# Kernel tuning notes

Hardware: AMD Instinct MI355X
Metric: run time of the kernel (lower is better)

Reference implementation:

```python
import jax, jax.numpy as jnp
import numpy as np
import math

B, L, IN, HID, NLAYERS, AA = 16, 512, 512, 512, 6, 21
KAPPA_ADD = 5.0


def _sru_layer(x, W, v, b):
    # x: [L, B, din]; W: [din, 2*HID*k]; v, b: [2(gate f/r), 2(dir), HID]
    Lx, Bx, din = x.shape
    d = HID
    k = W.shape[1] // (2 * d)  # 4 if projecting residual, 3 if residual = input
    U = (x @ W).reshape(Lx, Bx, 2, d, k)
    res = U[..., 3] if k == 4 else x.reshape(Lx, Bx, 2, d)
    # time-flip direction 1 so a single scan handles both directions
    flip = lambda a: jnp.concatenate([a[:, :, :1], a[::-1, :, 1:]], axis=2)
    u0, u1, u2, resf = flip(U[..., 0]), flip(U[..., 1]), flip(U[..., 2]), flip(res)
    vf, vr = v[0], v[1]
    bf, br = b[0], b[1]

    def step(c, t):
        u0t, u1t, u2t, rt = t
        f = jax.nn.sigmoid(u1t + vf * c + bf)
        c1 = f * c + (1.0 - f) * u0t
        r = jax.nn.sigmoid(u2t + vr * c1 + br)
        h = r * c1 + (1.0 - r) * rt
        return c1, h

    c0 = jnp.zeros((Bx, 2, d), x.dtype)
    _, H = jax.lax.scan(step, c0, (u0, u1, u2, resf))
    return flip(H).reshape(Lx, Bx, 2 * d)


def setup_inputs():
    key = jax.random.key(0)
    inp = {}
    inp['input'] = jax.random.normal(jax.random.fold_in(key, 0), (B, L, IN), jnp.float32)
    inp['hidden'] = jnp.zeros((NLAYERS, B, 2 * HID), jnp.float32)
    for l in range(NLAYERS):
        din = IN if l == 0 else 2 * HID
        k = 4 if din != 2 * HID else 3
        inp[f'sru_w{l}'] = jax.random.normal(jax.random.fold_in(key, 10 + l), (din, 2 * HID * k), jnp.float32) * (1.0 / math.sqrt(din))
        inp[f'sru_v{l}'] = jax.random.normal(jax.random.fold_in(key, 20 + l), (2, 2, HID), jnp.float32) * 0.1
        inp[f'sru_b{l}'] = jnp.zeros((2, 2, HID), jnp.float32)

    def lin(seed, din, dout):
        w = jax.random.normal(jax.random.fold_in(key, seed), (din, dout), jnp.float32) * (1.0 / math.sqrt(din))
        return w, jnp.zeros((dout,), jnp.float32)

    inp['fc1_logits_w'], inp['fc1_logits_b'] = lin(30, 2 * HID, HID)
    inp['fc2_logits_w'], inp['fc2_logits_b'] = lin(31, HID, AA)
    inp['fc1_angles_w'], inp['fc1_angles_b'] = lin(32, 2 * HID, HID)
    inp['fc2_means_w'], inp['fc2_means_b'] = lin(33, HID, 2)
    inp['fc2_kappas_w'], inp['fc2_kappas_b'] = lin(34, HID, 2)
    return inp


def reference(input, hidden, sru_w0, sru_v0, sru_b0, sru_w1, sru_v1, sru_b1, sru_w2, sru_v2, sru_b2, sru_w3, sru_v3, sru_b3, sru_w4, sru_v4, sru_b4, sru_w5, sru_v5, sru_b5, fc1_logits_w, fc1_logits_b, fc2_logits_w, fc2_logits_b, fc1_angles_w, fc1_angles_b, fc2_means_w, fc2_means_b, fc2_kappas_w, fc2_kappas_b):
    x = input.transpose(1, 0, 2)  # [L, B, IN]
    ws = [sru_w0, sru_w1, sru_w2, sru_w3, sru_w4, sru_w5]
    vs = [sru_v0, sru_v1, sru_v2, sru_v3, sru_v4, sru_v5]
    bs = [sru_b0, sru_b1, sru_b2, sru_b3, sru_b4, sru_b5]
    for W, v, b in zip(ws, vs, bs):
        x = _sru_layer(x, W, v, b)
    sru_out = x.transpose(1, 0, 2)  # [B, L, 2*HID]
    h_log = sru_out @ fc1_logits_w + fc1_logits_b
    output_logits = jax.nn.log_softmax(h_log @ fc2_logits_w + fc2_logits_b, axis=-1)
    h_ang = sru_out @ fc1_angles_w + fc1_angles_b
    output_means = jnp.tanh(h_ang @ fc2_means_w + fc2_means_b) * math.pi
    output_kappas = KAPPA_ADD + jax.nn.softplus(h_ang @ fc2_kappas_w + fc2_kappas_b)
    return (output_logits, output_means, output_kappas)
```

## Files before the change

### kernel.cpp

```cpp
#include <hip/hip_runtime.h>

typedef __attribute__((ext_vector_type(8))) short short8;
typedef __attribute__((ext_vector_type(4))) float f32x4;

__device__ __forceinline__ ushort f2bf(float x) {
  unsigned u = __builtin_bit_cast(unsigned, x);
  u = (u + 0x7fffu + ((u >> 16) & 1u)) >> 16;
  return (ushort)u;
}
__device__ __forceinline__ float bf2f(ushort x) {
  return __builtin_bit_cast(float, ((unsigned)x) << 16);
}

#define AS1CP(p) ((const __attribute__((address_space(1))) unsigned int*)(p))
#define AS3CP(p) ((__attribute__((address_space(3))) unsigned int*)(p))
#define GLDS(g, l, SZ) __builtin_amdgcn_global_load_lds(AS1CP(g), AS3CP(l), SZ, 0, 0)

__global__ __launch_bounds__(256) void k_cvt(const float* __restrict__ in,
                                             ushort* __restrict__ out, int n4) {
  int i = blockIdx.x * 256 + threadIdx.x;
  if (i >= n4) return;
  float4 v = reinterpret_cast<const float4*>(in)[i];
  ushort4 o;
  o.x = f2bf(v.x); o.y = f2bf(v.y); o.z = f2bf(v.z); o.w = f2bf(v.w);
  reinterpret_cast<ushort4*>(out)[i] = o;
}

__global__ __launch_bounds__(256) void k_transpose(const float* __restrict__ W,
                                                   ushort* __restrict__ Wt,
                                                   int N, int K) {
  __shared__ float tile[32][33];
  int bx = blockIdx.x * 32;
  int by = blockIdx.y * 32;
  int tx = threadIdx.x, ty = threadIdx.y;
#pragma unroll
  for (int i = 0; i < 32; i += 8)
    tile[ty + i][tx] = W[(size_t)(by + ty + i) * N + bx + tx];
  __syncthreads();
#pragma unroll
  for (int i = 0; i < 32; i += 8)
    Wt[(size_t)(bx + ty + i) * K + by + tx] = f2bf(tile[tx][ty + i]);
}

template <int BF16OUT>
__global__ __launch_bounds__(256) void k_gemm(const ushort* __restrict__ A,
                                              const ushort* __restrict__ Bt,
                                              void* __restrict__ Cv,
                                              int K, int N) {
  __shared__ __align__(16) ushort lsA[2][4096];
  __shared__ __align__(16) ushort lsB[2][4096];
  const int tid = threadIdx.x;
  const int bm = blockIdx.x, bn = blockIdx.y;
  const int w = tid >> 6, l = tid & 63;
  const int wm = (w >> 1) * 64, wn = (w & 1) * 64;
  const int lr = l & 15, lg = l >> 4;
  f32x4 acc[4][4] = {};
  const int srow = tid >> 2;
  const int scol = (((tid & 3) ^ ((srow >> 1) & 3))) * 8;
  const ushort* Ag = A + (size_t)(bm * 128 + srow) * K + scol;
  const ushort* Bg = Bt + (size_t)(bn * 128 + srow) * K + scol;
  const int nt = K >> 5;
  const int rxor = (lr >> 1) & 3;

#define GEMM_ISSUE(BUF, KT)                                       \
  {                                                               \
    GLDS(Ag + (KT), &lsA[BUF][w * 512], 16);                      \
    GLDS(Ag + (size_t)64 * K + (KT), &lsA[BUF][2048 + w * 512], 16); \
    GLDS(Bg + (KT), &lsB[BUF][w * 512], 16);                      \
    GLDS(Bg + (size_t)64 * K + (KT), &lsB[BUF][2048 + w * 512], 16); \
  }

  GEMM_ISSUE(0, 0);
  for (int t = 0; t < nt; ++t) {
    const int cur = t & 1;
    if (t + 1 < nt) {
      GEMM_ISSUE(cur ^ 1, (t + 1) * 32);
      asm volatile("s_waitcnt vmcnt(4)" ::: "memory");
    } else {
      asm volatile("s_waitcnt vmcnt(0)" ::: "memory");
    }
    asm volatile("s_barrier" ::: "memory");
    short8 af[4], bfr[4];
#pragma unroll
    for (int i = 0; i < 4; ++i)
      af[i] = *(const short8*)&lsA[cur][(wm + i * 16 + lr) * 32 + ((lg ^ rxor) * 8)];
#pragma unroll
    for (int j = 0; j < 4; ++j)
      bfr[j] = *(const short8*)&lsB[cur][(wn + j * 16 + lr) * 32 + ((lg ^ rxor) * 8)];
#pragma unroll
    for (int i = 0; i < 4; ++i)
#pragma unroll
      for (int j = 0; j < 4; ++j)
        acc[i][j] = __builtin_amdgcn_mfma_f32_16x16x32_bf16(af[i], bfr[j], acc[i][j], 0, 0, 0);
    asm volatile("s_barrier" ::: "memory");
  }
#undef GEMM_ISSUE
  const size_t cbase = (size_t)(bm * 128 + wm + lg * 4) * N + bn * 128 + wn + lr;
  if (BF16OUT) {
    ushort* Cb = (ushort*)Cv + cbase;
#pragma unroll
    for (int i = 0; i < 4; ++i)
#pragma unroll
      for (int j = 0; j < 4; ++j)
#pragma unroll
        for (int r = 0; r < 4; ++r)
          Cb[(size_t)(i * 16 + r) * N + j * 16] = f2bf(acc[i][j][r]);
  } else {
    float* Cb = (float*)Cv + cbase;
#pragma unroll
    for (int i = 0; i < 4; ++i)
#pragma unroll
      for (int j = 0; j < 4; ++j)
#pragma unroll
        for (int r = 0; r < 4; ++r)
          Cb[(size_t)(i * 16 + r) * N + j * 16] = acc[i][j][r];
  }
}

template <int KK>
__global__ __launch_bounds__(64, 1) void sru_rec5(const float* __restrict__ U,
                                                  const ushort* __restrict__ Xres,
                                                  const float* __restrict__ v,
                                                  const float* __restrict__ bb,
                                                  ushort* __restrict__ H) {
  const int lane = threadIdx.x;
  if (lane >= 16) return;
  const int blk = blockIdx.x;
  const int b = blk >> 6, rem = blk & 63, dir = rem >> 5, c0 = (rem & 31) << 4;
  const int h = c0 + lane;
  const float vf = v[dir * 512 + h], vr = v[1024 + dir * 512 + h];
  const float bfv = bb[dir * 512 + h], brv = bb[1024 + dir * 512 + h];
  const float vfn = -vf, vrn = -vr;
  const float kf0 = -bfv, kr0 = -brv;
  const int rs = 1024 * KK;
  const int tstep = dir ? -1 : 1;
  const int t0 = dir ? 511 : 0;
  const float* Ub = U + (size_t)b * 512 * rs + dir * 512 * KK + (size_t)h * KK;
  const ushort* Xb = Xres + (size_t)b * 512 * 1024 + dir * 512 + h;
  ushort* Hb = H + (size_t)b * 512 * 1024 + dir * 512 + h;

  float4 r4[4][8];
  float3 r3[4][8];
  ushort xr[4][8];

#define SR_ISSUE(J, TI)                                                        \
  {                                                                            \
    const int base_ = (TI) * 8;                                                \
    _Pragma("unroll")                                                          \
    for (int t = 0; t < 8; ++t) {                                              \
      int tt = t0 + tstep * (base_ + t);                                       \
      if (KK == 4) {                                                           \
        r4[J][t] = *(const float4*)(Ub + (size_t)tt * rs);                     \
      } else {                                                                 \
        r3[J][t] = *(const float3*)(Ub + (size_t)tt * rs);                     \
        xr[J][t] = Xb[(size_t)tt * 1024];                                      \
      }                                                                        \
    }                                                                          \
  }

#define SR_COMP(J, TI)                                                         \
  {                                                                            \
    _Pragma("unroll")                                                          \
    for (int s = 0; s < 8; ++s) {                                              \
      float u0, u1, u2, uR;                                                    \
      if (KK == 4) {                                                           \
        u0 = r4[J][s].x; u1 = r4[J][s].y; u2 = r4[J][s].z; uR = r4[J][s].w;    \
      } else {                                                                 \
        u0 = r3[J][s].x; u1 = r3[J][s].y; u2 = r3[J][s].z; uR = bf2f(xr[J][s]);\
      }                                                                        \
      float ef = __expf(__builtin_fmaf(vfn, c, kf0 - u1));                     \
      float f = __builtin_amdgcn_rcpf(1.f + ef);                               \
      c = __builtin_fmaf(f, c - u0, u0);                                       \
      float er = __expf(__builtin_fmaf(vrn, c, kr0 - u2));                     \
      float r = __builtin_amdgcn_rcpf(1.f + er);                               \
      float hh = __builtin_fmaf(r, c - uR, uR);                                \
      Hb[(size_t)(t0 + tstep * ((TI) * 8 + s)) * 1024] = f2bf(hh);             \
    }                                                                          \
  }

#define SR_WAIT                                                                \
  {                                                                            \
    if (KK == 3) asm volatile("s_waitcnt vmcnt(32)" ::: "memory");             \
    else         asm volatile("s_waitcnt vmcnt(16)" ::: "memory");             \
  }

  SR_ISSUE(0, 0)
  SR_ISSUE(1, 1)
  SR_ISSUE(2, 2)

  float c = 0.f;
#pragma unroll 1
  for (int ii = 0; ii < 15; ++ii) {
#define TILE_J(J)                                                              \
    {                                                                          \
      const int i = ii * 4 + (J);                                              \
      SR_WAIT                                                                  \
      SR_ISSUE((((J) + 3) & 3), i + 3)                                         \
      SR_COMP(J, i)                                                            \
    }
    TILE_J(0) TILE_J(1) TILE_J(2) TILE_J(3)
#undef TILE_J
  }
  SR_WAIT SR_ISSUE(3, 63) SR_COMP(0, 60)
  SR_WAIT SR_COMP(1, 61)
  SR_WAIT SR_COMP(2, 62)
  asm volatile("s_waitcnt vmcnt(0)" ::: "memory");
  SR_COMP(3, 63)
#undef SR_ISSUE
#undef SR_COMP
#undef SR_WAIT
}

__global__ __launch_bounds__(256) void k_buildW2(const float* __restrict__ w2l,
                                                 const float* __restrict__ w2m,
                                                 const float* __restrict__ w2k,
                                                 ushort* __restrict__ Wt2) {
  int i = blockIdx.x * 256 + threadIdx.x;
  if (i >= 128 * 1024) return;
  int n = i >> 10, k = i & 1023;
  float vv = 0.f;
  if (n < 21 && k < 512) vv = w2l[k * 21 + n];
  else if (n >= 21 && n < 23 && k >= 512) vv = w2m[(k - 512) * 2 + (n - 21)];
  else if (n >= 23 && n < 25 && k >= 512) vv = w2k[(k - 512) * 2 + (n - 23)];
  Wt2[i] = f2bf(vv);
}

__global__ __launch_bounds__(64) void k_bias25(const float* __restrict__ b1l,
                                               const float* __restrict__ b1a,
                                               const float* __restrict__ w2l,
                                               const float* __restrict__ b2l,
                                               const float* __restrict__ w2m,
                                               const float* __restrict__ b2m,
                                               const float* __restrict__ w2k,
                                               const float* __restrict__ b2k,
                                               float* __restrict__ b2adj) {
  int o = threadIdx.x;
  if (o >= 25) return;
  float s;
  if (o < 21) {
    s = b2l[o];
    for (int k = 0; k < 512; ++k) s += b1l[k] * w2l[k * 21 + o];
  } else if (o < 23) {
    s = b2m[o - 21];
    for (int k = 0; k < 512; ++k) s += b1a[k] * w2m[k * 2 + (o - 21)];
  } else {
    s = b2k[o - 23];
    for (int k = 0; k < 512; ++k) s += b1a[k] * w2k[k * 2 + (o - 23)];
  }
  b2adj[o] = s;
}

__global__ __launch_bounds__(64) void k_act(const float* __restrict__ T,
                                            const float* __restrict__ b2adj,
                                            float* __restrict__ out) {
  const int row = blockIdx.x;
  const int lane = threadIdx.x;
  float myv = 0.f;
  if (lane < 25) myv = T[(size_t)row * 128 + lane] + b2adj[lane];
  float x = (lane < 21) ? myv : -1e30f;
#pragma unroll
  for (int off = 32; off; off >>= 1) x = fmaxf(x, __shfl_xor(x, off));
  float e = (lane < 21) ? expf(myv - x) : 0.f;
#pragma unroll
  for (int off = 32; off; off >>= 1) e += __shfl_xor(e, off);
  float lse = x + logf(e);
  if (lane < 21) {
    out[(size_t)row * 21 + lane] = myv - lse;
  } else if (lane < 23) {
    out[172032 + row * 2 + (lane - 21)] = tanhf(myv) * 3.14159265358979323846f;
  } else if (lane < 25) {
    float sp = (myv > 20.f) ? myv : log1pf(expf(myv));
    out[188416 + row * 2 + (lane - 23)] = 5.f + sp;
  }
}

extern "C" void kernel_launch(void* const* d_in, const int* in_sizes, int n_in,
                              void* d_out, int out_size, void* d_ws, size_t ws_size,
                              hipStream_t stream) {
  (void)in_sizes; (void)n_in; (void)out_size; (void)ws_size;
  const float* input = (const float*)d_in[0];
  const float* sw[6]; const float* sv[6]; const float* sb[6];
  for (int l = 0; l < 6; ++l) {
    sw[l] = (const float*)d_in[2 + 3 * l];
    sv[l] = (const float*)d_in[3 + 3 * l];
    sb[l] = (const float*)d_in[4 + 3 * l];
  }
  const float* fc1lw = (const float*)d_in[20];
  const float* fc1lb = (const float*)d_in[21];
  const float* fc2lw = (const float*)d_in[22];
  const float* fc2lb = (const float*)d_in[23];
  const float* fc1aw = (const float*)d_in[24];
  const float* fc1ab = (const float*)d_in[25];
  const float* fc2mw = (const float*)d_in[26];
  const float* fc2mb = (const float*)d_in[27];
  const float* fc2kw = (const float*)d_in[28];
  const float* fc2kb = (const float*)d_in[29];

  char* ws = (char*)d_ws;
  float* U = (float*)ws;
  ushort* Hcat2 = (ushort*)ws;
  float* T = (float*)(ws + 67108864);
  ushort* H0 = (ushort*)(ws + 134217728);
  ushort* H1 = (ushort*)(ws + 150994944);
  ushort* X0 = (ushort*)(ws + 167772160);
  const size_t wbase = 176160768;
  ushort* Wtl[6];
  Wtl[0] = (ushort*)(ws + wbase);
  for (int l = 1; l < 6; ++l)
    Wtl[l] = (ushort*)(ws + wbase + 4194304 + (size_t)(l - 1) * 6291456);
  ushort* Wfc = (ushort*)(ws + wbase + 4194304 + 5ull * 6291456);
  ushort* Wt2 = (ushort*)(ws + wbase + 37748736);
  float* b2adj = (float*)(ws + wbase + 38010880);

  k_cvt<<<4096, 256, 0, stream>>>(input, X0, 8192 * 512 / 4);
  k_buildW2<<<512, 256, 0, stream>>>(fc2lw, fc2mw, fc2kw, Wt2);
  k_bias25<<<1, 64, 0, stream>>>(fc1lb, fc1ab, fc2lw, fc2lb, fc2mw, fc2mb,
                                 fc2kw, fc2kb, b2adj);

  k_transpose<<<dim3(4096 / 32, 512 / 32), dim3(32, 8), 0, stream>>>(sw[0], Wtl[0], 4096, 512);
  for (int l = 1; l < 6; ++l)
    k_transpose<<<dim3(3072 / 32, 1024 / 32), dim3(32, 8), 0, stream>>>(sw[l], Wtl[l], 3072, 1024);
  k_transpose<<<dim3(512 / 32, 1024 / 32), dim3(32, 8), 0, stream>>>(fc1lw, Wfc, 512, 1024);
  k_transpose<<<dim3(512 / 32, 1024 / 32), dim3(32, 8), 0, stream>>>(fc1aw, Wfc + (size_t)512 * 1024, 512, 1024);

  for (int l = 0; l < 6; ++l) {
    const ushort* Ain = (l == 0) ? X0 : ((l & 1) ? H0 : H1);
    ushort* Hout = (l & 1) ? H1 : H0;
    int K = (l == 0) ? 512 : 1024;
    int N = (l == 0) ? 4096 : 3072;
    k_gemm<0><<<dim3(64, N / 128), 256, 0, stream>>>(Ain, Wtl[l], U, K, N);
    if (l == 0)
      sru_rec5<4><<<1024, 64, 0, stream>>>(U, X0 , sv[l], sb[l], Hout);
    else
      sru_rec5<3><<<1024, 64, 0, stream>>>(U, Ain, sv[l], sb[l], Hout);
  }

  k_gemm<1><<<dim3(64, 8), 256, 0, stream>>>(H1, Wfc, Hcat2, 1024, 1024);

  k_gemm<0><<<dim3(64, 1), 256, 0, stream>>>(Hcat2, Wt2, T, 1024, 128);

  k_act<<<8192, 64, 0, stream>>>(T, b2adj, (float*)d_out);
}
```

Measured before the change: 808.5 us.

## Store SRU projections in bf16 with gate-planar column layout and retune prefetch depth

The layer GEMMs now write their U output in bf16 instead of fp32. The weight transpose permutes output columns so u0/u1 sit interleaved, u2 and the residual projection are planar, which lets the recurrence load u0/u1 as one 32-bit word. The recurrence kernel is rewritten to read these bf16 planes, and its prefetch distance drops from three tiles to two. This halves GEMM store and recurrence load traffic, at the cost of bf16 rounding on the pre-activation values and more, smaller load instructions per step.

```diff
diff --git a/kernel.cpp b/kernel.cpp
--- a/kernel.cpp
+++ b/kernel.cpp
@@ -40,6 +40,27 @@
 #pragma unroll
   for (int i = 0; i < 32; i += 8)
     Wt[(size_t)(bx + ty + i) * K + by + tx] = f2bf(tile[tx][ty + i]);
+}
+
+template <int KKp>
+__global__ __launch_bounds__(256) void k_transpose_sru(const float* __restrict__ W,
+                                                       ushort* __restrict__ Wt,
+                                                       int N, int K) {
+  __shared__ float tile[32][33];
+  int bx = blockIdx.x * 32;
+  int by = blockIdx.y * 32;
+  int tx = threadIdx.x, ty = threadIdx.y;
+#pragma unroll
+  for (int i = 0; i < 32; i += 8)
+    tile[ty + i][tx] = W[(size_t)(by + ty + i) * N + bx + tx];
+  __syncthreads();
+#pragma unroll
+  for (int i = 0; i < 32; i += 8) {
+    int c = bx + ty + i;
+    int ch = c / KKp, j = c - ch * KKp;
+    int nc = (j < 2) ? (ch * 2 + j) : ((j == 2) ? (2048 + ch) : (3072 + ch));
+    Wt[(size_t)nc * K + by + tx] = f2bf(tile[tx][ty + i]);
+  }
 }
 
 template <int BF16OUT>
@@ -117,31 +138,29 @@
   }
 }
 
-template <int KK>
-__global__ __launch_bounds__(64, 1) void sru_rec5(const float* __restrict__ U,
-                                                  const ushort* __restrict__ Xres,
+__global__ __launch_bounds__(64, 1) void sru_rec6(const ushort* __restrict__ U, int NU,
+                                                  const ushort* __restrict__ R, int RS,
                                                   const float* __restrict__ v,
                                                   const float* __restrict__ bb,
                                                   ushort* __restrict__ H) {
   const int lane = threadIdx.x;
   if (lane >= 16) return;
   const int blk = blockIdx.x;
-  const int b = blk >> 6, rem = blk & 63, dir = rem >> 5, c0 = (rem & 31) << 4;
-  const int h = c0 + lane;
-  const float vf = v[dir * 512 + h], vr = v[1024 + dir * 512 + h];
-  const float bfv = bb[dir * 512 + h], brv = bb[1024 + dir * 512 + h];
+  const int b = blk >> 6, rem = blk & 63, dir = rem >> 5;
+  const int ch = dir * 512 + ((rem & 31) << 4) + lane;
+  const float vf = v[ch], vr = v[1024 + ch];
+  const float bfv = bb[ch], brv = bb[1024 + ch];
   const float vfn = -vf, vrn = -vr;
   const float kf0 = -bfv, kr0 = -brv;
-  const int rs = 1024 * KK;
   const int tstep = dir ? -1 : 1;
   const int t0 = dir ? 511 : 0;
-  const float* Ub = U + (size_t)b * 512 * rs + dir * 512 * KK + (size_t)h * KK;
-  const ushort* Xb = Xres + (size_t)b * 512 * 1024 + dir * 512 + h;
-  ushort* Hb = H + (size_t)b * 512 * 1024 + dir * 512 + h;
-
-  float4 r4[4][8];
-  float3 r3[4][8];
-  ushort xr[4][8];
+  const ushort* U01 = U + (size_t)b * 512 * NU + ch * 2;
+  const ushort* U2  = U + (size_t)b * 512 * NU + 2048 + ch;
+  const ushort* Rb  = R + (size_t)b * 512 * RS + ch;
+  ushort* Hb = H + (size_t)b * 512 * 1024 + ch;
+
+  unsigned q01[4][8];
+  ushort q2[4][8], qr[4][8];
 
 #define SR_ISSUE(J, TI)                                                        \
   {                                                                            \
@@ -149,12 +168,9 @@
     _Pragma("unroll")                                                          \
     for (int t = 0; t < 8; ++t) {                                              \
       int tt = t0 + tstep * (base_ + t);                                       \
-      if (KK == 4) {                                                           \
-        r4[J][t] = *(const float4*)(Ub + (size_t)tt * rs);                     \
-      } else {                                                                 \
-        r3[J][t] = *(const float3*)(Ub + (size_t)tt * rs);                     \
-        xr[J][t] = Xb[(size_t)tt * 1024];                                      \
-      }                                                                        \
+      q01[J][t] = *(const unsigned*)(U01 + (size_t)tt * NU);                   \
+      q2[J][t] = U2[(size_t)tt * NU];                                          \
+      qr[J][t] = Rb[(size_t)tt * RS];                                          \
     }                                                                          \
   }
 
@@ -162,12 +178,10 @@
   {                                                                            \
     _Pragma("unroll")                                                          \
     for (int s = 0; s < 8; ++s) {                                              \
-      float u0, u1, u2, uR;                                                    \
-      if (KK == 4) {                                                           \
-        u0 = r4[J][s].x; u1 = r4[J][s].y; u2 = r4[J][s].z; uR = r4[J][s].w;    \
-      } else {                                                                 \
-        u0 = r3[J][s].x; u1 = r3[J][s].y; u2 = r3[J][s].z; uR = bf2f(xr[J][s]);\
-      }                                                                        \
+      float u0 = bf2f((ushort)(q01[J][s] & 0xffffu));                          \
+      float u1 = bf2f((ushort)(q01[J][s] >> 16));                              \
+      float u2 = bf2f(q2[J][s]);                                               \
+      float uR = bf2f(qr[J][s]);                                               \
       float ef = __expf(__builtin_fmaf(vfn, c, kf0 - u1));                     \
       float f = __builtin_amdgcn_rcpf(1.f + ef);                               \
       c = __builtin_fmaf(f, c - u0, u0);                                       \
@@ -178,37 +192,36 @@
     }                                                                          \
   }
 
-#define SR_WAIT                                                                \
-  {                                                                            \
-    if (KK == 3) asm volatile("s_waitcnt vmcnt(32)" ::: "memory");             \
-    else         asm volatile("s_waitcnt vmcnt(16)" ::: "memory");             \
-  }
+#define SR_W32 asm volatile("s_waitcnt vmcnt(32)" ::: "memory");
 
   SR_ISSUE(0, 0)
   SR_ISSUE(1, 1)
-  SR_ISSUE(2, 2)
-
   float c = 0.f;
+  asm volatile("s_waitcnt vmcnt(24)" ::: "memory");
+  SR_ISSUE(2, 2) SR_COMP(0, 0)
+  SR_W32 SR_ISSUE(3, 3) SR_COMP(1, 1)
+  SR_W32 SR_ISSUE(0, 4) SR_COMP(2, 2)
+  SR_W32 SR_ISSUE(1, 5) SR_COMP(3, 3)
 #pragma unroll 1
-  for (int ii = 0; ii < 15; ++ii) {
+  for (int ii = 1; ii <= 14; ++ii) {
 #define TILE_J(J)                                                              \
     {                                                                          \
       const int i = ii * 4 + (J);                                              \
-      SR_WAIT                                                                  \
-      SR_ISSUE((((J) + 3) & 3), i + 3)                                         \
+      SR_W32                                                                   \
+      SR_ISSUE((((J) + 2) & 3), i + 2)                                         \
       SR_COMP(J, i)                                                            \
     }
     TILE_J(0) TILE_J(1) TILE_J(2) TILE_J(3)
 #undef TILE_J
   }
-  SR_WAIT SR_ISSUE(3, 63) SR_COMP(0, 60)
-  SR_WAIT SR_COMP(1, 61)
-  SR_WAIT SR_COMP(2, 62)
-  asm volatile("s_waitcnt vmcnt(0)" ::: "memory");
+  SR_W32 SR_ISSUE(2, 62) SR_COMP(0, 60)
+  SR_W32 SR_ISSUE(3, 63) SR_COMP(1, 61)
+  SR_W32 SR_COMP(2, 62)
+  asm volatile("s_waitcnt vmcnt(8)" ::: "memory");
   SR_COMP(3, 63)
 #undef SR_ISSUE
 #undef SR_COMP
-#undef SR_WAIT
+#undef SR_W32
 }
 
 __global__ __launch_bounds__(256) void k_buildW2(const float* __restrict__ w2l,
@@ -297,7 +310,7 @@
   const float* fc2kb = (const float*)d_in[29];
 
   char* ws = (char*)d_ws;
-  float* U = (float*)ws;
+  ushort* U = (ushort*)ws;
   ushort* Hcat2 = (ushort*)ws;
   float* T = (float*)(ws + 67108864);
   ushort* H0 = (ushort*)(ws + 134217728);
@@ -317,22 +330,22 @@
   k_bias25<<<1, 64, 0, stream>>>(fc1lb, fc1ab, fc2lw, fc2lb, fc2mw, fc2mb,
                                  fc2kw, fc2kb, b2adj);
 
-  k_transpose<<<dim3(4096 / 32, 512 / 32), dim3(32, 8), 0, stream>>>(sw[0], Wtl[0], 4096, 512);
+  k_transpose_sru<4><<<dim3(128, 16), dim3(32, 8), 0, stream>>>(sw[0], Wtl[0], 4096, 512);
   for (int l = 1; l < 6; ++l)
-    k_transpose<<<dim3(3072 / 32, 1024 / 32), dim3(32, 8), 0, stream>>>(sw[l], Wtl[l], 3072, 1024);
-  k_transpose<<<dim3(512 / 32, 1024 / 32), dim3(32, 8), 0, stream>>>(fc1lw, Wfc, 512, 1024);
-  k_transpose<<<dim3(512 / 32, 1024 / 32), dim3(32, 8), 0, stream>>>(fc1aw, Wfc + (size_t)512 * 1024, 512, 1024);
+    k_transpose_sru<3><<<dim3(96, 32), dim3(32, 8), 0, stream>>>(sw[l], Wtl[l], 3072, 1024);
+  k_transpose<<<dim3(16, 32), dim3(32, 8), 0, stream>>>(fc1lw, Wfc, 512, 1024);
+  k_transpose<<<dim3(16, 32), dim3(32, 8), 0, stream>>>(fc1aw, Wfc + (size_t)512 * 1024, 512, 1024);
 
   for (int l = 0; l < 6; ++l) {
     const ushort* Ain = (l == 0) ? X0 : ((l & 1) ? H0 : H1);
     ushort* Hout = (l & 1) ? H1 : H0;
     int K = (l == 0) ? 512 : 1024;
     int N = (l == 0) ? 4096 : 3072;
-    k_gemm<0><<<dim3(64, N / 128), 256, 0, stream>>>(Ain, Wtl[l], U, K, N);
+    k_gemm<1><<<dim3(64, N / 128), 256, 0, stream>>>(Ain, Wtl[l], U, K, N);
     if (l == 0)
-      sru_rec5<4><<<1024, 64, 0, stream>>>(U, X0 , sv[l], sb[l], Hout);
+      sru_rec6<<<1024, 64, 0, stream>>>(U, 4096, U + 3072, 4096, sv[l], sb[l], Hout);
     else
-      sru_rec5<3><<<1024, 64, 0, stream>>>(U, Ain, sv[l], sb[l], Hout);
+      sru_rec6<<<1024, 64, 0, stream>>>(U, 3072, Ain, 1024, sv[l], sb[l], Hout);
   }
 
   k_gemm<1><<<dim3(64, 8), 256, 0, stream>>>(H1, Wfc, Hcat2, 1024, 1024);
```

Result: slower. 886.1 us (+9.6%).
